# Kernel optimization log

Hardware: AMD Instinct MI355X
Metric: run time of the kernel (lower is better)

Reference implementation:

```python
import jax, jax.numpy as jnp
import numpy as np

B, N, D = 4, 1024, 1024
H, DK, DV = 8, 128, 128
EPS = 1e-6


def setup_inputs() -> dict:
    key = jax.random.key(0)
    ks = jax.random.split(key, 16)
    s = 0.02
    return {
        "q_time": jax.random.normal(ks[0], (B, N, D), jnp.float32),
        "k_time": jax.random.normal(ks[1], (B, N, D), jnp.float32),
        "q_feature": jax.random.normal(ks[2], (B, N, D), jnp.float32),
        "k_feature": jax.random.normal(ks[3], (B, N, D), jnp.float32),
        "v": jax.random.normal(ks[4], (B, N, D), jnp.float32),
        "attn_mask": jax.random.randint(ks[5], (B, N, N), 0, 2, jnp.int32),
        "w_qs_time": jax.random.normal(ks[6], (H * DK, D), jnp.float32) * s,
        "w_ks_time": jax.random.normal(ks[7], (H * DK, D), jnp.float32) * s,
        "w_qs_feature": jax.random.normal(ks[8], (H * DV, D), jnp.float32) * s,
        "w_ks_feature": jax.random.normal(ks[9], (H * DV, D), jnp.float32) * s,
        "w_vs": jax.random.normal(ks[10], (H * DV, D), jnp.float32) * s,
        "w_fc": jax.random.normal(ks[11], (D, H * DV), jnp.float32) * s,
        "ln_gamma": jnp.ones((D,), jnp.float32),
        "ln_beta": jnp.zeros((D,), jnp.float32),
    }


def reference(q_time, k_time, q_feature, k_feature, v, attn_mask,
              w_qs_time, w_ks_time, w_qs_feature, w_ks_feature, w_vs,
              w_fc, ln_gamma, ln_beta):
    temp = DK ** 0.5
    residual = v

    def proj(x, w, d):
        # [B,N,D] @ [D, H*d] -> [B,H,N,d]
        return (x @ w.T).reshape(B, N, H, d).transpose(0, 2, 1, 3)

    qt = proj(q_time, w_qs_time, DK)
    kt = proj(k_time, w_ks_time, DK)
    qf = proj(q_feature, w_qs_feature, DV)
    kf = proj(k_feature, w_ks_feature, DV)
    vv = proj(v, w_vs, DV)

    # time attention: [B,H,N,N]
    attn_time = jnp.einsum('bhnd,bhmd->bhnm', qt / temp, kt)
    attn_time = jnp.where(attn_mask[:, None, :, :] == 0, -1e9, attn_time)
    attn_time = jax.nn.softmax(attn_time, axis=-1)

    # feature attention: q_feature^T @ k_feature -> [B,H,DV,DV]
    attn_feature = jnp.einsum('bhnd,bhne->bhde', qf / temp, kf)
    attn_feature = jax.nn.softmax(attn_feature, axis=-1)

    # chained matmuls: (attn_time @ v) @ attn_feature -> [B,H,N,DV]
    out = jnp.einsum('bhnm,bhmd->bhnd', attn_time, vv)
    out = jnp.einsum('bhnd,bhde->bhne', out, attn_feature)

    out = out.transpose(0, 2, 1, 3).reshape(B, N, H * DV)
    out = out @ w_fc.T + residual  # dropout = identity (eval)

    mean = jnp.mean(out, axis=-1, keepdims=True)
    var = jnp.var(out, axis=-1, keepdims=True)
    out = (out - mean) / jnp.sqrt(var + EPS) * ln_gamma + ln_beta
    return out, attn_time, attn_feature
```

## Files before the change

### kernel.cpp

```cpp
#include <hip/hip_runtime.h>
#include <hip/hip_bf16.h>
#include <cstdint>
#include <cstddef>

typedef unsigned short u16;
typedef unsigned int u32;
typedef short v8s __attribute__((ext_vector_type(8)));
typedef float v4f __attribute__((ext_vector_type(4)));
typedef __hip_bfloat16 bf16;

#define PROJ_ELEMS  4194304ull
#define AT_ELEMS    33554432ull
#define INV_TEMP    0.08838834764831845f

#define GLOBAL_AS __attribute__((address_space(1)))
#define LDS_AS    __attribute__((address_space(3)))

__device__ __forceinline__ void store_out(float* p, float v) { *p = v; }
__device__ __forceinline__ void store_out(bf16* p, float v) { *p = __float2bfloat16(v); }

__device__ __forceinline__ v8s load8f(const float* p) {
    const float4 a = *(const float4*)p;
    const float4 b = *(const float4*)(p + 4);
    v8s r;
    bf16 t;
    t = __float2bfloat16(a.x); r[0] = *(const short*)&t;
    t = __float2bfloat16(a.y); r[1] = *(const short*)&t;
    t = __float2bfloat16(a.z); r[2] = *(const short*)&t;
    t = __float2bfloat16(a.w); r[3] = *(const short*)&t;
    t = __float2bfloat16(b.x); r[4] = *(const short*)&t;
    t = __float2bfloat16(b.y); r[5] = *(const short*)&t;
    t = __float2bfloat16(b.z); r[6] = *(const short*)&t;
    t = __float2bfloat16(b.w); r[7] = *(const short*)&t;
    return r;
}

template <typename AT, typename OutT>
__device__ __forceinline__ void gemm_core(
    const AT* __restrict__ Ab, const u16* __restrict__ Bb, OutT* __restrict__ Cb,
    int K, int lda, int ldb, int ldc, float alpha, int m0, int n0)
{
    __shared__ __align__(16) u16 sA[128][32];
    __shared__ __align__(16) u16 sB[128][32];

    const int tid  = threadIdx.x;
    const int lane = tid & 63;
    const int wid  = tid >> 6;
    const int wm = (wid >> 1) * 64;
    const int wn = (wid & 1) * 64;
    const int quad = lane >> 4;
    const int l16  = lane & 15;

    v4f acc[4][4];
    #pragma unroll
    for (int i = 0; i < 4; ++i)
        #pragma unroll
        for (int j = 0; j < 4; ++j)
            acc[i][j] = (v4f){0.f, 0.f, 0.f, 0.f};

    for (int k0 = 0; k0 < K; k0 += 32) {
        #pragma unroll
        for (int it = 0; it < 2; ++it) {
            const int slot = tid + it * 256;
            const int row  = slot >> 2;
            const int cg   = (slot & 3) << 3;
            __builtin_amdgcn_global_load_lds(
                (const GLOBAL_AS void*)(Bb + (size_t)(n0 + row) * (size_t)ldb + (size_t)(k0 + cg)),
                (LDS_AS void*)((char*)&sB[0][0] + slot * 16), 16, 0, 0);
            if constexpr (sizeof(AT) == 2) {
                __builtin_amdgcn_global_load_lds(
                    (const GLOBAL_AS void*)((const u16*)Ab + (size_t)(m0 + row) * (size_t)lda + (size_t)(k0 + cg)),
                    (LDS_AS void*)((char*)&sA[0][0] + slot * 16), 16, 0, 0);
            } else {
                *(v8s*)&sA[row][cg] =
                    load8f((const float*)Ab + (size_t)(m0 + row) * (size_t)lda + (size_t)(k0 + cg));
            }
        }
        __syncthreads();

        v8s af[4], bfr[4];
        #pragma unroll
        for (int i = 0; i < 4; ++i) {
            af[i]  = *(const v8s*)&sA[wm + i * 16 + l16][quad * 8];
            bfr[i] = *(const v8s*)&sB[wn + i * 16 + l16][quad * 8];
        }
        #pragma unroll
        for (int i = 0; i < 4; ++i)
            #pragma unroll
            for (int j = 0; j < 4; ++j)
                acc[i][j] = __builtin_amdgcn_mfma_f32_16x16x32_bf16(af[i], bfr[j], acc[i][j], 0, 0, 0);
        __syncthreads();
    }

    #pragma unroll
    for (int i = 0; i < 4; ++i) {
        int rbase = m0 + wm + i * 16 + quad * 4;
        #pragma unroll
        for (int j = 0; j < 4; ++j) {
            int gcol = n0 + wn + j * 16 + l16;
            #pragma unroll
            for (int r = 0; r < 4; ++r)
                store_out(&Cb[(size_t)(rbase + r) * (size_t)ldc + (size_t)gcol],
                          acc[i][j][r] * alpha);
        }
    }
}

template <typename AT, typename OutT>
__global__ __launch_bounds__(256, 3)
void gemm_fast(const AT* __restrict__ A, const u16* __restrict__ B, OutT* __restrict__ C,
               int K, int lda, int ldb, int ldc, int batDiv,
               long long sAo, long long sAi, long long sBo, long long sBi,
               long long sCo, long long sCi, float alpha, int swz)
{
    const int z  = blockIdx.z;
    const int zo = z / batDiv;
    const int zi = z - zo * batDiv;
    int bx, by;
    if (swz) {
        const int flat = blockIdx.x + (blockIdx.y << 3);
        const int xcd = flat & 7, slt = flat >> 3;
        by = xcd + ((slt >> 3) << 3);
        bx = slt & 7;
    } else {
        bx = blockIdx.x; by = blockIdx.y;
    }
    gemm_core<AT, OutT>(A + (size_t)zo * (size_t)sAo + (size_t)zi * (size_t)sAi,
                        B + (size_t)zo * (size_t)sBo + (size_t)zi * (size_t)sBi,
                        C + (size_t)zo * (size_t)sCo + (size_t)zi * (size_t)sCi,
                        K, lda, ldb, ldc, alpha, by * 128, bx * 128);
}

struct P5 { const u16* a[5]; };
__global__ __launch_bounds__(256, 3)
void gemm_proj5(P5 As, const u16* __restrict__ W, u16* __restrict__ C)
{
    const int fid = blockIdx.x + (blockIdx.y << 3) + (blockIdx.z << 8);
    const int xcd = fid & 7, s = fid >> 3;
    const int p = ((s >> 3) << 3) + xcd;
    const int bx = s & 7;
    const int by = p & 31;
    const int z  = p >> 5;
    gemm_core<u16, bf16>(As.a[z], W + (size_t)z * 1048576ull,
                         (bf16*)(C + (size_t)z * PROJ_ELEMS),
                         1024, 1024, 1024, 1024, 1.f, by * 128, bx * 128);
}

__global__ __launch_bounds__(256, 3)
void gemm_feat_sk(const u16* __restrict__ qfT, const u16* __restrict__ kfT, float* __restrict__ Fp)
{
    const int kc = blockIdx.x, z = blockIdx.y;
    gemm_core<u16, float>(qfT + (size_t)z * 131072ull + (size_t)kc * 128ull,
                          kfT + (size_t)z * 131072ull + (size_t)kc * 128ull,
                          Fp + ((size_t)kc * 32 + z) * 16384ull,
                          128, 1024, 1024, 128, INV_TEMP, 0, 0);
}

struct CP11 { const float* p[11]; };

__global__ __launch_bounds__(256)
void cvt_all(CP11 ps, u16* __restrict__ actDst, u16* __restrict__ wDst)
{
    const int z = blockIdx.z;
    const int nblk = (z < 5) ? 2048 : 512;
    if (blockIdx.x >= nblk) return;
    const float* s = ps.p[z];
    u16* d = (z < 5) ? (actDst + (size_t)z * PROJ_ELEMS)
                     : (wDst + (size_t)(z - 5) * 1048576ull);
    const int i = (blockIdx.x * 256 + threadIdx.x) * 8;
    *(v8s*)(d + i) = load8f(s + i);
}

__global__ __launch_bounds__(256)
void mask_pack(const int* __restrict__ mask, u32* __restrict__ mb)
{
    const int w = blockIdx.x * 256 + threadIdx.x;
    const int* src = mask + (size_t)w * 32ull;
    u32 bits = 0;
    #pragma unroll
    for (int i = 0; i < 32; i += 4) {
        int4 v = *(const int4*)(src + i);
        bits |= (u32)(v.x != 0) << i;
        bits |= (u32)(v.y != 0) << (i + 1);
        bits |= (u32)(v.z != 0) << (i + 2);
        bits |= (u32)(v.w != 0) << (i + 3);
    }
    mb[w] = bits;
}

struct T3 { const u16* in[3]; u16* out[3]; };
__global__ __launch_bounds__(256)
void transpose3(T3 t3)
{
    __shared__ u16 tile[32][33];
    const int sel = blockIdx.z >> 5;
    const int z   = blockIdx.z & 31;
    const int b = z >> 3, h = z & 7;
    const u16* ib = t3.in[sel] + (size_t)b * 1048576ull + (size_t)h * 128ull;
    u16* ob = t3.out[sel] + (size_t)z * 131072ull;
    const int m0 = blockIdx.x * 32;
    const int d0 = blockIdx.y * 32;
    const int tx = threadIdx.x;
    const int ty = threadIdx.y;
    #pragma unroll
    for (int i = 0; i < 4; ++i)
        tile[ty + i * 8][tx] = ib[(size_t)(m0 + ty + i * 8) * 1024ull + (size_t)(d0 + tx)];
    __syncthreads();
    #pragma unroll
    for (int i = 0; i < 4; ++i)
        ob[(size_t)(d0 + ty + i * 8) * 1024ull + (size_t)(m0 + tx)] = tile[tx][ty + i * 8];
}

__global__ __launch_bounds__(512, 2)
void fused_attn(const u16* __restrict__ qt, const u16* __restrict__ kt,
                const u16* __restrict__ vvT, const u32* __restrict__ mb,
                float* __restrict__ oAT, u16* __restrict__ opv)
{
    __shared__ __align__(16) u16 sQ[4][128][32];
    __shared__ __align__(16) u16 sT[2][4][128][32];
    __shared__ __align__(16) u16 sP[4][128][40];
    __shared__ u32 smw[2][128][4];

    const int flat = blockIdx.x + (blockIdx.y << 3);
    const int xcd = flat & 7, slt = flat >> 3;
    const int z  = xcd + ((slt >> 3) << 3);
    const int m0 = (slt & 7) << 7;

    const int b = z >> 3, h = z & 7;
    const u16* qb = qt + (size_t)b * 1048576ull + (size_t)h * 128ull;
    const u16* kb = kt + (size_t)b * 1048576ull + (size_t)h * 128ull;
    const u16* vb = vvT + (size_t)z * 131072ull;
    float* Ob = oAT + (size_t)z * 1048576ull;
    const u32* mbb = mb + (size_t)b * 32768ull;

    const int tid = threadIdx.x;
    const int lane = tid & 63, wid = tid >> 6;
    const int quad = lane >> 4, l16 = lane & 15;
    const int wm = wid << 4;

    auto stK = [&](int nt, int buf) {
        #pragma unroll
        for (int it = 0; it < 4; ++it) {
            const int s2 = tid + it * 512;
            const int ks = s2 >> 9, row = (s2 >> 2) & 127, cg = (s2 & 3) << 3;
            __builtin_amdgcn_global_load_lds(
                (const GLOBAL_AS void*)(kb + (size_t)(nt * 128 + row) * 1024ull + ks * 32 + cg),
                (LDS_AS void*)((char*)&sT[buf][0][0][0] + s2 * 16), 16, 0, 0);
        }
    };
    auto stV = [&](int nt, int buf) {
        #pragma unroll
        for (int it = 0; it < 4; ++it) {
            const int s2 = tid + it * 512;
            const int ks = s2 >> 9, row = (s2 >> 2) & 127, cg = (s2 & 3) << 3;
            __builtin_amdgcn_global_load_lds(
                (const GLOBAL_AS void*)(vb + (size_t)row * 1024ull + nt * 128 + ks * 32 + cg),
                (LDS_AS void*)((char*)&sT[buf][0][0][0] + s2 * 16), 16, 0, 0);
        }
    };
    auto stM = [&](int nt, int buf) {
        const int W = tid;
        __builtin_amdgcn_global_load_lds(
            (const GLOBAL_AS void*)(mbb + (size_t)(m0 + (W >> 2)) * 32ull + nt * 4 + (W & 3)),
            (LDS_AS void*)((char*)&smw[buf][0][0] + W * 4), 4, 0, 0);
    };

    #pragma unroll
    for (int it = 0; it < 4; ++it) {
        const int s2 = tid + it * 512;
        const int ks = s2 >> 9, row = (s2 >> 2) & 127, cg = (s2 & 3) << 3;
        __builtin_amdgcn_global_load_lds(
            (const GLOBAL_AS void*)(qb + (size_t)(m0 + row) * 1024ull + ks * 32 + cg),
            (LDS_AS void*)((char*)&sQ[0][0][0] + s2 * 16), 16, 0, 0);
    }
    stK(0, 0); stM(0, 0);

    float Mreg[4], Lreg[4];
    #pragma unroll
    for (int x = 0; x < 4; ++x) { Mreg[x] = -3.0e38f; Lreg[x] = 0.f; }

    int bufA = 0, mcur = 0;
    for (int nt = 0; nt < 8; ++nt) {
        stK((nt + 1) & 7, bufA ^ 1);
        stM((nt + 1) & 7, mcur ^ 1);
        asm volatile("s_waitcnt vmcnt(5)" ::: "memory");
        __builtin_amdgcn_s_barrier();
        __builtin_amdgcn_sched_barrier(0);

        v4f acc[8];
        #pragma unroll
        for (int j = 0; j < 8; ++j)
            acc[j] = (v4f){0.f, 0.f, 0.f, 0.f};
        #pragma unroll
        for (int ks = 0; ks < 4; ++ks) {
            const v8s aq = *(const v8s*)&sQ[ks][wm + l16][quad * 8];
            v8s bk[8];
            #pragma unroll
            for (int j = 0; j < 8; ++j)
                bk[j] = *(const v8s*)&sT[bufA][ks][j * 16 + l16][quad * 8];
            #pragma unroll
            for (int j = 0; j < 8; ++j)
                acc[j] = __builtin_amdgcn_mfma_f32_16x16x32_bf16(aq, bk[j], acc[j], 0, 0, 0);
        }

        #pragma unroll
        for (int r = 0; r < 4; ++r) {
            const int rowl = wm + quad * 4 + r;
            const u32 mw0 = smw[mcur][rowl][0];
            const u32 mw1 = smw[mcur][rowl][1];
            const u32 mw2 = smw[mcur][rowl][2];
            const u32 mw3 = smw[mcur][rowl][3];
            float sv[8];
            float tmax = -3.0e38f;
            #pragma unroll
            for (int j = 0; j < 8; ++j) {
                const u32 word = (j < 2) ? mw0 : (j < 4) ? mw1 : (j < 6) ? mw2 : mw3;
                const int bit = ((j & 1) << 4) + l16;
                float s = acc[j][r] * INV_TEMP;
                s = ((word >> bit) & 1u) ? s : -1e9f;
                sv[j] = s;
                tmax = fmaxf(tmax, s);
            }
            #pragma unroll
            for (int m = 1; m <= 8; m <<= 1)
                tmax = fmaxf(tmax, __shfl_xor(tmax, m));
            const float Mo = Mreg[r];
            const float Mn = fmaxf(Mo, tmax);
            float t = 0.f;
            #pragma unroll
            for (int j = 0; j < 8; ++j)
                t += __expf(sv[j] - Mn);
            #pragma unroll
            for (int m = 1; m <= 8; m <<= 1)
                t += __shfl_xor(t, m);
            Lreg[r] = Lreg[r] * __expf(Mo - Mn) + t;
            Mreg[r] = Mn;
        }

        asm volatile("s_waitcnt lgkmcnt(0)" ::: "memory");
        __builtin_amdgcn_s_barrier();
        __builtin_amdgcn_sched_barrier(0);
        bufA ^= 1; mcur ^= 1;
    }

    float IL[4];
    #pragma unroll
    for (int x = 0; x < 4; ++x) IL[x] = 1.f / Lreg[x];

    const int BK = bufA;
    const int BV = BK ^ 1;

    v4f pacc[8];
    #pragma unroll
    for (int j = 0; j < 8; ++j)
        pacc[j] = (v4f){0.f, 0.f, 0.f, 0.f};

    for (int nt = 0; nt < 8; ++nt) {
        stV(nt, BV);
        if (nt == 0) {
            asm volatile("s_waitcnt vmcnt(4)" ::: "memory");
        } else {
            asm volatile("s_waitcnt vmcnt(36)" ::: "memory");
        }
        __builtin_amdgcn_s_barrier();
        __builtin_amdgcn_sched_barrier(0);

        v4f acc[8];
        #pragma unroll
        for (int j = 0; j < 8; ++j)
            acc[j] = (v4f){0.f, 0.f, 0.f, 0.f};
        #pragma unroll
        for (int ks = 0; ks < 4; ++ks) {
            const v8s aq = *(const v8s*)&sQ[ks][wm + l16][quad * 8];
            v8s bk[8];
            #pragma unroll
            for (int j = 0; j < 8; ++j)
                bk[j] = *(const v8s*)&sT[BK][ks][j * 16 + l16][quad * 8];
            #pragma unroll
            for (int j = 0; j < 8; ++j)
                acc[j] = __builtin_amdgcn_mfma_f32_16x16x32_bf16(aq, bk[j], acc[j], 0, 0, 0);
        }

        asm volatile("s_waitcnt lgkmcnt(0)" ::: "memory");
        __builtin_amdgcn_s_barrier();
        __builtin_amdgcn_sched_barrier(0);

        if (nt < 7) {
            stK(nt + 1, BK);
            stM(nt + 1, mcur ^ 1);
            asm volatile("s_waitcnt vmcnt(5)" ::: "memory");
        } else {
            asm volatile("s_waitcnt vmcnt(0)" ::: "memory");
        }

        #pragma unroll
        for (int r = 0; r < 4; ++r) {
            const int rowl = wm + quad * 4 + r;
            const u32 mw0 = smw[mcur][rowl][0];
            const u32 mw1 = smw[mcur][rowl][1];
            const u32 mw2 = smw[mcur][rowl][2];
            const u32 mw3 = smw[mcur][rowl][3];
            float* orow = Ob + (size_t)(m0 + rowl) * 1024ull + nt * 128;
            #pragma unroll
            for (int j = 0; j < 8; ++j) {
                const u32 word = (j < 2) ? mw0 : (j < 4) ? mw1 : (j < 6) ? mw2 : mw3;
                const int bit = ((j & 1) << 4) + l16;
                float s = acc[j][r] * INV_TEMP;
                s = ((word >> bit) & 1u) ? s : -1e9f;
                const float p = __expf(s - Mreg[r]) * IL[r];
                orow[j * 16 + l16] = p;
                bf16 pb = __float2bfloat16(p);
                sP[j >> 1][rowl][((j & 1) << 4) + l16] = *(const u16*)&pb;
            }
        }

        asm volatile("s_waitcnt lgkmcnt(0)" ::: "memory");
        __builtin_amdgcn_s_barrier();
        __builtin_amdgcn_sched_barrier(0);

        #pragma unroll
        for (int ks = 0; ks < 4; ++ks) {
            const v8s ap = *(const v8s*)&sP[ks][wm + l16][quad * 8];
            v8s bv[8];
            #pragma unroll
            for (int j = 0; j < 8; ++j)
                bv[j] = *(const v8s*)&sT[BV][ks][j * 16 + l16][quad * 8];
            #pragma unroll
            for (int j = 0; j < 8; ++j)
                pacc[j] = __builtin_amdgcn_mfma_f32_16x16x32_bf16(ap, bv[j], pacc[j], 0, 0, 0);
        }

        asm volatile("s_waitcnt lgkmcnt(0)" ::: "memory");
        __builtin_amdgcn_s_barrier();
        __builtin_amdgcn_sched_barrier(0);
        mcur ^= 1;
    }

    u16* opvB = opv + (size_t)z * 131072ull;
    const int rbase = m0 + wm + quad * 4;
    #pragma unroll
    for (int j = 0; j < 8; ++j) {
        const int e = j * 16 + l16;
        #pragma unroll
        for (int r = 0; r < 4; ++r) {
            bf16 t = __float2bfloat16(pacc[j][r]);
            opvB[(size_t)(rbase + r) * 128ull + e] = *(const u16*)&t;
        }
    }
}

__global__ __launch_bounds__(128)
void softmax_feat(const float* __restrict__ Fp, float* __restrict__ out_af, u16* __restrict__ FT)
{
    const int r = blockIdx.x;
    const int z = r >> 7, d = r & 127;
    const int e = threadIdx.x;
    float x = 0.f;
    #pragma unroll
    for (int kc = 0; kc < 8; ++kc)
        x += Fp[((size_t)kc * 32 + z) * 16384ull + (size_t)d * 128ull + e];
    float mx = x;
    #pragma unroll
    for (int o = 32; o; o >>= 1) mx = fmaxf(mx, __shfl_xor(mx, o));
    __shared__ float redm[2], reds[2];
    const int w = e >> 6;
    if ((e & 63) == 0) redm[w] = mx;
    __syncthreads();
    mx = fmaxf(redm[0], redm[1]);
    float ex = __expf(x - mx);
    float s = ex;
    #pragma unroll
    for (int o = 32; o; o >>= 1) s += __shfl_xor(s, o);
    if ((e & 63) == 0) reds[w] = s;
    __syncthreads();
    s = reds[0] + reds[1];
    float p = ex / s;
    out_af[(size_t)r * 128ull + e] = p;
    bf16 pb = __float2bfloat16(p);
    FT[(size_t)z * 16384ull + (size_t)e * 128ull + d] = *(const u16*)&pb;
}

__global__ __launch_bounds__(256)
void resid_ln(const float* __restrict__ fc, const float* __restrict__ v,
              const float* __restrict__ gamma, const float* __restrict__ beta,
              float* __restrict__ out)
{
    const int r = blockIdx.x;
    const int t = threadIdx.x;
    const float4* fr = (const float4*)(fc + (size_t)r * 1024ull);
    const float4* vr = (const float4*)(v  + (size_t)r * 1024ull);
    float4 a = fr[t], b4 = vr[t];
    float4 x = {a.x + b4.x, a.y + b4.y, a.z + b4.z, a.w + b4.w};
    float s  = x.x + x.y + x.z + x.w;
    float s2 = x.x * x.x + x.y * x.y + x.z * x.z + x.w * x.w;
    #pragma unroll
    for (int o = 32; o; o >>= 1) { s += __shfl_xor(s, o); s2 += __shfl_xor(s2, o); }
    __shared__ float rs[4], rs2[4];
    const int w = t >> 6;
    if ((t & 63) == 0) { rs[w] = s; rs2[w] = s2; }
    __syncthreads();
    s  = rs[0] + rs[1] + rs[2] + rs[3];
    s2 = rs2[0] + rs2[1] + rs2[2] + rs2[3];
    const float mean = s * (1.f / 1024.f);
    const float var  = s2 * (1.f / 1024.f) - mean * mean;
    const float rstd = rsqrtf(var + 1e-6f);
    const float4 g = ((const float4*)gamma)[t];
    const float4 bb = ((const float4*)beta)[t];
    float4 o4 = {(x.x - mean) * rstd * g.x + bb.x,
                 (x.y - mean) * rstd * g.y + bb.y,
                 (x.z - mean) * rstd * g.z + bb.z,
                 (x.w - mean) * rstd * g.w + bb.w};
    ((float4*)(out + (size_t)r * 1024ull))[t] = o4;
}

extern "C" void kernel_launch(void* const* d_in, const int* in_sizes, int n_in,
                              void* d_out, int out_size, void* d_ws, size_t ws_size,
                              hipStream_t stream)
{
    (void)in_sizes; (void)n_in; (void)out_size; (void)ws_size;
    const float* q_time    = (const float*)d_in[0];
    const float* k_time    = (const float*)d_in[1];
    const float* q_feature = (const float*)d_in[2];
    const float* k_feature = (const float*)d_in[3];
    const float* v_in      = (const float*)d_in[4];
    const int*   mask      = (const int*)d_in[5];
    const float* w_qs_t    = (const float*)d_in[6];
    const float* w_ks_t    = (const float*)d_in[7];
    const float* w_qs_f    = (const float*)d_in[8];
    const float* w_ks_f    = (const float*)d_in[9];
    const float* w_vs      = (const float*)d_in[10];
    const float* w_fc      = (const float*)d_in[11];
    const float* gamma     = (const float*)d_in[12];
    const float* beta      = (const float*)d_in[13];

    char* ws = (char*)d_ws;
    const size_t MB = 1ull << 20;
    u16*   act = (u16*)(ws + 0  * MB);
    u16*   wbf = (u16*)(ws + 40 * MB);
    u16*   qt  = (u16*)(ws + 52 * MB);
    u16*   vvT = (u16*)(ws + 0  * MB);
    u16*   qfT = (u16*)(ws + 8  * MB);
    u16*   kfT = (u16*)(ws + 16 * MB);
    u16*   FT  = (u16*)(ws + 24 * MB);
    float* Fp  = (float*)(ws + 25 * MB);
    u16*   opv = (u16*)(ws + 41 * MB);
    u16*   o2  = (u16*)(ws + 52 * MB);
    float* fc  = (float*)(ws + 60 * MB);
    u32*   mb  = (u32*)(ws + 92 * MB);
    u16*   kt  = qt + PROJ_ELEMS;
    u16*   qf  = kt + PROJ_ELEMS;
    u16*   kf  = qf + PROJ_ELEMS;
    u16*   vv  = kf + PROJ_ELEMS;
    u16*   wfc = wbf + 5ull * 1048576ull;

    float* out0 = (float*)d_out;
    float* oAT  = out0 + PROJ_ELEMS;
    float* oAF  = out0 + PROJ_ELEMS + AT_ELEMS;

    const dim3 blk(256);

    {
        CP11 ca;
        ca.p[0] = q_time; ca.p[1] = k_time; ca.p[2] = q_feature;
        ca.p[3] = k_feature; ca.p[4] = v_in;
        ca.p[5] = w_qs_t; ca.p[6] = w_ks_t; ca.p[7] = w_qs_f;
        ca.p[8] = w_ks_f; ca.p[9] = w_vs; ca.p[10] = w_fc;
        cvt_all<<<dim3(2048, 1, 11), blk, 0, stream>>>(ca, act, wbf);
        mask_pack<<<512, blk, 0, stream>>>(mask, mb);
    }

    {
        P5 ps; for (int i = 0; i < 5; ++i) ps.a[i] = act + (size_t)i * PROJ_ELEMS;
        gemm_proj5<<<dim3(8, 32, 5), blk, 0, stream>>>(ps, wbf, qt);
    }

    {
        T3 t3; t3.in[0] = vv; t3.in[1] = qf; t3.in[2] = kf;
               t3.out[0] = vvT; t3.out[1] = qfT; t3.out[2] = kfT;
        transpose3<<<dim3(32, 4, 96), dim3(32, 8, 1), 0, stream>>>(t3);
    }

    gemm_feat_sk<<<dim3(8, 32), blk, 0, stream>>>(qfT, kfT, Fp);

    softmax_feat<<<4096, 128, 0, stream>>>(Fp, oAF, FT);

    fused_attn<<<dim3(8, 32), dim3(512), 0, stream>>>(qt, kt, vvT, mb, oAT, opv);

    gemm_fast<<<dim3(1, 8, 32), blk, 0, stream>>>(opv, FT, (bf16*)o2, 128,
        128, 128, 1024, 8, 1048576LL, 131072LL, 131072LL, 16384LL, 1048576LL, 128LL, 1.f, 0);

    gemm_fast<<<dim3(8, 32, 1), blk, 0, stream>>>(o2, wfc, fc, 1024, 1024, 1024, 1024, 1,
        0LL, 0LL, 0LL, 0LL, 0LL, 0LL, 1.f, 1);

    resid_ln<<<4096, 256, 0, stream>>>(fc, v_in, gamma, beta, out0);
}
```

Baseline: 441.8 us.

## Fuse feature-attention matmul into attention kernel with smaller 64-row tiles

The fused attention kernel now uses 256-thread blocks over 64 query rows and 64-key tiles, doubling the block count. After the PV accumulation it multiplies by the feature-softmax matrix in-kernel (swizzled LDS tile) and writes o2 directly, removing a separate batched GEMM launch and the opv round trip. It also folds mask packing into the conversion kernel to save a launch. The second pass now waits for all loads (vmcnt(0)) each iteration, which may reduce load/compute overlap, and recomputes QK for more, smaller tiles.

New measurement: 446.4 us. Within noise of the previous version (+1.0%).

```diff
diff --git a/kernel.cpp b/kernel.cpp
--- a/kernel.cpp
+++ b/kernel.cpp
@@ -159,9 +159,26 @@
 struct CP11 { const float* p[11]; };
 
 __global__ __launch_bounds__(256)
-void cvt_all(CP11 ps, u16* __restrict__ actDst, u16* __restrict__ wDst)
+void cvt_all(CP11 ps, u16* __restrict__ actDst, u16* __restrict__ wDst,
+             const int* __restrict__ mask, u32* __restrict__ mb)
 {
     const int z = blockIdx.z;
+    if (z == 11) {
+        if (blockIdx.x >= 512) return;
+        const int w = blockIdx.x * 256 + threadIdx.x;
+        const int* src = mask + (size_t)w * 32ull;
+        u32 bits = 0;
+        #pragma unroll
+        for (int i = 0; i < 32; i += 4) {
+            int4 v = *(const int4*)(src + i);
+            bits |= (u32)(v.x != 0) << i;
+            bits |= (u32)(v.y != 0) << (i + 1);
+            bits |= (u32)(v.z != 0) << (i + 2);
+            bits |= (u32)(v.w != 0) << (i + 3);
+        }
+        mb[w] = bits;
+        return;
+    }
     const int nblk = (z < 5) ? 2048 : 512;
     if (blockIdx.x >= nblk) return;
     const float* s = ps.p[z];
@@ -169,23 +186,6 @@
                      : (wDst + (size_t)(z - 5) * 1048576ull);
     const int i = (blockIdx.x * 256 + threadIdx.x) * 8;
     *(v8s*)(d + i) = load8f(s + i);
-}
-
-__global__ __launch_bounds__(256)
-void mask_pack(const int* __restrict__ mask, u32* __restrict__ mb)
-{
-    const int w = blockIdx.x * 256 + threadIdx.x;
-    const int* src = mask + (size_t)w * 32ull;
-    u32 bits = 0;
-    #pragma unroll
-    for (int i = 0; i < 32; i += 4) {
-        int4 v = *(const int4*)(src + i);
-        bits |= (u32)(v.x != 0) << i;
-        bits |= (u32)(v.y != 0) << (i + 1);
-        bits |= (u32)(v.z != 0) << (i + 2);
-        bits |= (u32)(v.w != 0) << (i + 3);
-    }
-    mb[w] = bits;
 }
 
 struct T3 { const u16* in[3]; u16* out[3]; };
@@ -211,20 +211,21 @@
         ob[(size_t)(d0 + ty + i * 8) * 1024ull + (size_t)(m0 + tx)] = tile[tx][ty + i * 8];
 }
 
-__global__ __launch_bounds__(512, 2)
+__global__ __launch_bounds__(256, 2)
 void fused_attn(const u16* __restrict__ qt, const u16* __restrict__ kt,
                 const u16* __restrict__ vvT, const u32* __restrict__ mb,
-                float* __restrict__ oAT, u16* __restrict__ opv)
-{
-    __shared__ __align__(16) u16 sQ[4][128][32];
-    __shared__ __align__(16) u16 sT[2][4][128][32];
-    __shared__ __align__(16) u16 sP[4][128][40];
-    __shared__ u32 smw[2][128][4];
-
-    const int flat = blockIdx.x + (blockIdx.y << 3);
-    const int xcd = flat & 7, slt = flat >> 3;
-    const int z  = xcd + ((slt >> 3) << 3);
-    const int m0 = (slt & 7) << 7;
+                const u16* __restrict__ FTg,
+                float* __restrict__ oAT, u16* __restrict__ o2)
+{
+    __shared__ __align__(16) u16 sQ[4][64][32];
+    __shared__ __align__(16) u16 sT2[2][8192];
+    __shared__ __align__(16) u16 sP[2][64][40];
+    __shared__ u32 smw[2][64][2];
+
+    const int flat = blockIdx.x + (blockIdx.y << 4);
+    const int xcd = flat & 7, s = flat >> 3;
+    const int z  = xcd + ((s >> 4) << 3);
+    const int m0 = (s & 15) << 6;
 
     const int b = z >> 3, h = z & 7;
     const u16* qb = qt + (size_t)b * 1048576ull + (size_t)h * 128ull;
@@ -241,34 +242,34 @@
     auto stK = [&](int nt, int buf) {
         #pragma unroll
         for (int it = 0; it < 4; ++it) {
-            const int s2 = tid + it * 512;
-            const int ks = s2 >> 9, row = (s2 >> 2) & 127, cg = (s2 & 3) << 3;
+            const int s2 = tid + it * 256;
+            const int ks = s2 >> 8, row = (s2 >> 2) & 63, cg = (s2 & 3) << 3;
             __builtin_amdgcn_global_load_lds(
-                (const GLOBAL_AS void*)(kb + (size_t)(nt * 128 + row) * 1024ull + ks * 32 + cg),
-                (LDS_AS void*)((char*)&sT[buf][0][0][0] + s2 * 16), 16, 0, 0);
+                (const GLOBAL_AS void*)(kb + (size_t)(nt * 64 + row) * 1024ull + ks * 32 + cg),
+                (LDS_AS void*)((char*)&sT2[buf][0] + s2 * 16), 16, 0, 0);
         }
     };
     auto stV = [&](int nt, int buf) {
         #pragma unroll
         for (int it = 0; it < 4; ++it) {
-            const int s2 = tid + it * 512;
-            const int ks = s2 >> 9, row = (s2 >> 2) & 127, cg = (s2 & 3) << 3;
+            const int s2 = tid + it * 256;
+            const int ks2 = s2 >> 9, row = (s2 >> 2) & 127, cg = (s2 & 3) << 3;
             __builtin_amdgcn_global_load_lds(
-                (const GLOBAL_AS void*)(vb + (size_t)row * 1024ull + nt * 128 + ks * 32 + cg),
-                (LDS_AS void*)((char*)&sT[buf][0][0][0] + s2 * 16), 16, 0, 0);
+                (const GLOBAL_AS void*)(vb + (size_t)row * 1024ull + nt * 64 + ks2 * 32 + cg),
+                (LDS_AS void*)((char*)&sT2[buf][0] + s2 * 16), 16, 0, 0);
         }
     };
     auto stM = [&](int nt, int buf) {
-        const int W = tid;
+        const int W = tid & 127;
         __builtin_amdgcn_global_load_lds(
-            (const GLOBAL_AS void*)(mbb + (size_t)(m0 + (W >> 2)) * 32ull + nt * 4 + (W & 3)),
+            (const GLOBAL_AS void*)(mbb + (size_t)(m0 + (W >> 1)) * 32ull + nt * 2 + (W & 1)),
             (LDS_AS void*)((char*)&smw[buf][0][0] + W * 4), 4, 0, 0);
     };
 
     #pragma unroll
     for (int it = 0; it < 4; ++it) {
-        const int s2 = tid + it * 512;
-        const int ks = s2 >> 9, row = (s2 >> 2) & 127, cg = (s2 & 3) << 3;
+        const int s2 = tid + it * 256;
+        const int ks = s2 >> 8, row = (s2 >> 2) & 63, cg = (s2 & 3) << 3;
         __builtin_amdgcn_global_load_lds(
             (const GLOBAL_AS void*)(qb + (size_t)(m0 + row) * 1024ull + ks * 32 + cg),
             (LDS_AS void*)((char*)&sQ[0][0][0] + s2 * 16), 16, 0, 0);
@@ -280,26 +281,26 @@
     for (int x = 0; x < 4; ++x) { Mreg[x] = -3.0e38f; Lreg[x] = 0.f; }
 
     int bufA = 0, mcur = 0;
-    for (int nt = 0; nt < 8; ++nt) {
-        stK((nt + 1) & 7, bufA ^ 1);
-        stM((nt + 1) & 7, mcur ^ 1);
+    for (int nt = 0; nt < 16; ++nt) {
+        stK((nt + 1) & 15, bufA ^ 1);
+        stM((nt + 1) & 15, mcur ^ 1);
         asm volatile("s_waitcnt vmcnt(5)" ::: "memory");
         __builtin_amdgcn_s_barrier();
         __builtin_amdgcn_sched_barrier(0);
 
-        v4f acc[8];
-        #pragma unroll
-        for (int j = 0; j < 8; ++j)
+        v4f acc[4];
+        #pragma unroll
+        for (int j = 0; j < 4; ++j)
             acc[j] = (v4f){0.f, 0.f, 0.f, 0.f};
         #pragma unroll
         for (int ks = 0; ks < 4; ++ks) {
             const v8s aq = *(const v8s*)&sQ[ks][wm + l16][quad * 8];
-            v8s bk[8];
-            #pragma unroll
-            for (int j = 0; j < 8; ++j)
-                bk[j] = *(const v8s*)&sT[bufA][ks][j * 16 + l16][quad * 8];
-            #pragma unroll
-            for (int j = 0; j < 8; ++j)
+            v8s bk[4];
+            #pragma unroll
+            for (int j = 0; j < 4; ++j)
+                bk[j] = *(const v8s*)&sT2[bufA][ks * 2048 + (j * 16 + l16) * 32 + quad * 8];
+            #pragma unroll
+            for (int j = 0; j < 4; ++j)
                 acc[j] = __builtin_amdgcn_mfma_f32_16x16x32_bf16(aq, bk[j], acc[j], 0, 0, 0);
         }
 
@@ -308,18 +309,16 @@
             const int rowl = wm + quad * 4 + r;
             const u32 mw0 = smw[mcur][rowl][0];
             const u32 mw1 = smw[mcur][rowl][1];
-            const u32 mw2 = smw[mcur][rowl][2];
-            const u32 mw3 = smw[mcur][rowl][3];
-            float sv[8];
+            float sv[4];
             float tmax = -3.0e38f;
             #pragma unroll
-            for (int j = 0; j < 8; ++j) {
-                const u32 word = (j < 2) ? mw0 : (j < 4) ? mw1 : (j < 6) ? mw2 : mw3;
+            for (int j = 0; j < 4; ++j) {
+                const u32 word = (j < 2) ? mw0 : mw1;
                 const int bit = ((j & 1) << 4) + l16;
-                float s = acc[j][r] * INV_TEMP;
-                s = ((word >> bit) & 1u) ? s : -1e9f;
-                sv[j] = s;
-                tmax = fmaxf(tmax, s);
+                float sc = acc[j][r] * INV_TEMP;
+                sc = ((word >> bit) & 1u) ? sc : -1e9f;
+                sv[j] = sc;
+                tmax = fmaxf(tmax, sc);
             }
             #pragma unroll
             for (int m = 1; m <= 8; m <<= 1)
@@ -328,7 +327,7 @@
             const float Mn = fmaxf(Mo, tmax);
             float t = 0.f;
             #pragma unroll
-            for (int j = 0; j < 8; ++j)
+            for (int j = 0; j < 4; ++j)
                 t += __expf(sv[j] - Mn);
             #pragma unroll
             for (int m = 1; m <= 8; m <<= 1)
@@ -343,54 +342,37 @@
         bufA ^= 1; mcur ^= 1;
     }
 
+    const int BK = 0, BV = 1;
+    stV(0, BV);
+
     float IL[4];
     #pragma unroll
     for (int x = 0; x < 4; ++x) IL[x] = 1.f / Lreg[x];
-
-    const int BK = bufA;
-    const int BV = BK ^ 1;
 
     v4f pacc[8];
     #pragma unroll
     for (int j = 0; j < 8; ++j)
         pacc[j] = (v4f){0.f, 0.f, 0.f, 0.f};
 
-    for (int nt = 0; nt < 8; ++nt) {
-        stV(nt, BV);
-        if (nt == 0) {
-            asm volatile("s_waitcnt vmcnt(4)" ::: "memory");
-        } else {
-            asm volatile("s_waitcnt vmcnt(36)" ::: "memory");
-        }
+    for (int nt = 0; nt < 16; ++nt) {
+        asm volatile("s_waitcnt vmcnt(0)" ::: "memory");
         __builtin_amdgcn_s_barrier();
         __builtin_amdgcn_sched_barrier(0);
 
-        v4f acc[8];
-        #pragma unroll
-        for (int j = 0; j < 8; ++j)
+        v4f acc[4];
+        #pragma unroll
+        for (int j = 0; j < 4; ++j)
             acc[j] = (v4f){0.f, 0.f, 0.f, 0.f};
         #pragma unroll
         for (int ks = 0; ks < 4; ++ks) {
             const v8s aq = *(const v8s*)&sQ[ks][wm + l16][quad * 8];
-            v8s bk[8];
-            #pragma unroll
-            for (int j = 0; j < 8; ++j)
-                bk[j] = *(const v8s*)&sT[BK][ks][j * 16 + l16][quad * 8];
-            #pragma unroll
-            for (int j = 0; j < 8; ++j)
+            v8s bk[4];
+            #pragma unroll
+            for (int j = 0; j < 4; ++j)
+                bk[j] = *(const v8s*)&sT2[BK][ks * 2048 + (j * 16 + l16) * 32 + quad * 8];
+            #pragma unroll
+            for (int j = 0; j < 4; ++j)
                 acc[j] = __builtin_amdgcn_mfma_f32_16x16x32_bf16(aq, bk[j], acc[j], 0, 0, 0);
-        }
-
-        asm volatile("s_waitcnt lgkmcnt(0)" ::: "memory");
-        __builtin_amdgcn_s_barrier();
-        __builtin_amdgcn_sched_barrier(0);
-
-        if (nt < 7) {
-            stK(nt + 1, BK);
-            stM(nt + 1, mcur ^ 1);
-            asm volatile("s_waitcnt vmcnt(5)" ::: "memory");
-        } else {
-            asm volatile("s_waitcnt vmcnt(0)" ::: "memory");
         }
 
         #pragma unroll
@@ -398,19 +380,18 @@
             const int rowl = wm + quad * 4 + r;
             const u32 mw0 = smw[mcur][rowl][0];
             const u32 mw1 = smw[mcur][rowl][1];
-            const u32 mw2 = smw[mcur][rowl][2];
-            const u32 mw3 = smw[mcur][rowl][3];
-            float* orow = Ob + (size_t)(m0 + rowl) * 1024ull + nt * 128;
-            #pragma unroll
-            for (int j = 0; j < 8; ++j) {
-                const u32 word = (j < 2) ? mw0 : (j < 4) ? mw1 : (j < 6) ? mw2 : mw3;
+            float* orow = Ob + (size_t)(m0 + rowl) * 1024ull + nt * 64;
+            #pragma unroll
+            for (int j = 0; j < 4; ++j) {
+                const u32 word = (j < 2) ? mw0 : mw1;
                 const int bit = ((j & 1) << 4) + l16;
-                float s = acc[j][r] * INV_TEMP;
-                s = ((word >> bit) & 1u) ? s : -1e9f;
-                const float p = __expf(s - Mreg[r]) * IL[r];
+                float sc = acc[j][r] * INV_TEMP;
+                sc = ((word >> bit) & 1u) ? sc : -1e9f;
+                const float p = __expf(sc - Mreg[r]) * IL[r];
                 orow[j * 16 + l16] = p;
                 bf16 pb = __float2bfloat16(p);
-                sP[j >> 1][rowl][((j & 1) << 4) + l16] = *(const u16*)&pb;
+                const int c = j * 16 + l16;
+                sP[c >> 5][rowl][c & 31] = *(const u16*)&pb;
             }
         }
 
@@ -418,13 +399,15 @@
         __builtin_amdgcn_s_barrier();
         __builtin_amdgcn_sched_barrier(0);
 
-        #pragma unroll
-        for (int ks = 0; ks < 4; ++ks) {
-            const v8s ap = *(const v8s*)&sP[ks][wm + l16][quad * 8];
+        if (nt < 15) { stK(nt + 1, BK); stM(nt + 1, mcur ^ 1); }
+
+        #pragma unroll
+        for (int ks2 = 0; ks2 < 2; ++ks2) {
+            const v8s ap = *(const v8s*)&sP[ks2][wm + l16][quad * 8];
             v8s bv[8];
             #pragma unroll
             for (int j = 0; j < 8; ++j)
-                bv[j] = *(const v8s*)&sT[BV][ks][j * 16 + l16][quad * 8];
+                bv[j] = *(const v8s*)&sT2[BV][ks2 * 4096 + (j * 16 + l16) * 32 + quad * 8];
             #pragma unroll
             for (int j = 0; j < 8; ++j)
                 pacc[j] = __builtin_amdgcn_mfma_f32_16x16x32_bf16(ap, bv[j], pacc[j], 0, 0, 0);
@@ -433,18 +416,61 @@
         asm volatile("s_waitcnt lgkmcnt(0)" ::: "memory");
         __builtin_amdgcn_s_barrier();
         __builtin_amdgcn_sched_barrier(0);
+
+        if (nt < 15) stV(nt + 1, BV);
         mcur ^= 1;
     }
 
-    u16* opvB = opv + (size_t)z * 131072ull;
-    const int rbase = m0 + wm + quad * 4;
+    u16* sPVp = &sQ[0][0][0];
+    u16* sFTp = &sT2[0][0];
+    const u16* FTz = FTg + (size_t)z * 16384ull;
+
     #pragma unroll
     for (int j = 0; j < 8; ++j) {
-        const int e = j * 16 + l16;
+        const int c = j * 16 + l16;
         #pragma unroll
         for (int r = 0; r < 4; ++r) {
-            bf16 t = __float2bfloat16(pacc[j][r]);
-            opvB[(size_t)(rbase + r) * 128ull + e] = *(const u16*)&t;
+            const int rowl = wm + quad * 4 + r;
+            bf16 pb = __float2bfloat16(pacc[j][r]);
+            sPVp[(c >> 5) * 2048 + rowl * 32 + (c & 31)] = *(const u16*)&pb;
+        }
+    }
+    #pragma unroll
+    for (int rep = 0; rep < 8; ++rep) {
+        const int grp = tid + rep * 256;
+        const int row = grp >> 4;
+        v8s v = *(const v8s*)(FTz + (size_t)grp * 8ull);
+        *(v8s*)((char*)sFTp + ((grp * 16) ^ ((row & 7) << 4))) = v;
+    }
+    asm volatile("s_waitcnt lgkmcnt(0)" ::: "memory");
+    __builtin_amdgcn_s_barrier();
+    __builtin_amdgcn_sched_barrier(0);
+
+    v4f o2a[8];
+    #pragma unroll
+    for (int j = 0; j < 8; ++j)
+        o2a[j] = (v4f){0.f, 0.f, 0.f, 0.f};
+    #pragma unroll
+    for (int ks = 0; ks < 4; ++ks) {
+        const v8s ap2 = *(const v8s*)&sPVp[ks * 2048 + (wm + l16) * 32 + quad * 8];
+        #pragma unroll
+        for (int j = 0; j < 8; ++j) {
+            const int rowf = j * 16 + l16;
+            const v8s bft = *(const v8s*)((char*)sFTp +
+                ((rowf * 256 + ks * 64 + quad * 16) ^ ((rowf & 7) << 4)));
+            o2a[j] = __builtin_amdgcn_mfma_f32_16x16x32_bf16(ap2, bft, o2a[j], 0, 0, 0);
+        }
+    }
+
+    u16* o2B = o2 + (size_t)b * 1048576ull + (size_t)h * 128ull;
+    #pragma unroll
+    for (int j = 0; j < 8; ++j) {
+        const int c = j * 16 + l16;
+        #pragma unroll
+        for (int r = 0; r < 4; ++r) {
+            const int m = m0 + wm + quad * 4 + r;
+            bf16 t = __float2bfloat16(o2a[j][r]);
+            o2B[(size_t)m * 1024ull + c] = *(const u16*)&t;
         }
     }
 }
@@ -543,8 +569,7 @@
     u16*   kfT = (u16*)(ws + 16 * MB);
     u16*   FT  = (u16*)(ws + 24 * MB);
     float* Fp  = (float*)(ws + 25 * MB);
-    u16*   opv = (u16*)(ws + 41 * MB);
-    u16*   o2  = (u16*)(ws + 52 * MB);
+    u16*   o2  = (u16*)(ws + 41 * MB);
     float* fc  = (float*)(ws + 60 * MB);
     u32*   mb  = (u32*)(ws + 92 * MB);
     u16*   kt  = qt + PROJ_ELEMS;
@@ -565,8 +590,7 @@
         ca.p[3] = k_feature; ca.p[4] = v_in;
         ca.p[5] = w_qs_t; ca.p[6] = w_ks_t; ca.p[7] = w_qs_f;
         ca.p[8] = w_ks_f; ca.p[9] = w_vs; ca.p[10] = w_fc;
-        cvt_all<<<dim3(2048, 1, 11), blk, 0, stream>>>(ca, act, wbf);
-        mask_pack<<<512, blk, 0, stream>>>(mask, mb);
+        cvt_all<<<dim3(2048, 1, 12), blk, 0, stream>>>(ca, act, wbf, mask, mb);
     }
 
     {
@@ -584,10 +608,7 @@
 
     softmax_feat<<<4096, 128, 0, stream>>>(Fp, oAF, FT);
 
-    fused_attn<<<dim3(8, 32), dim3(512), 0, stream>>>(qt, kt, vvT, mb, oAT, opv);
-
-    gemm_fast<<<dim3(1, 8, 32), blk, 0, stream>>>(opv, FT, (bf16*)o2, 128,
-        128, 128, 1024, 8, 1048576LL, 131072LL, 131072LL, 16384LL, 1048576LL, 128LL, 1.f, 0);
+    fused_attn<<<dim3(16, 32), blk, 0, stream>>>(qt, kt, vvT, mb, FT, oAT, o2);
 
     gemm_fast<<<dim3(8, 32, 1), blk, 0, stream>>>(o2, wfc, fc, 1024, 1024, 1024, 1024, 1,
         0LL, 0LL, 0LL, 0LL, 0LL, 0LL, 1.f, 1);
```

## Fuse feature-attention matmul into attention epilogue and merge mask packing into conversion

Applied to the files above, without the earlier changes.

The attention kernel's epilogue now stages its P@V tile in shared memory, loads the transposed feature-softmax matrix with an XOR swizzle, and runs the second chained matmul in place. It writes the result straight into the [B,N,H*DV] layout the FC GEMM reads. This removes one gemm_fast launch and the round trip of the opv intermediate through global memory. The mask bit-packing is also folded into the conversion kernel as an extra grid slice, which saves another launch. The cost is extra LDS traffic and a barrier at the end of the attention kernel, and it reuses the sQ/sT buffers after the main loop.

Result: no change. 434.3 us (-1.7%).

```diff
diff --git a/kernel.cpp b/kernel.cpp
--- a/kernel.cpp
+++ b/kernel.cpp
@@ -159,9 +159,26 @@
 struct CP11 { const float* p[11]; };
 
 __global__ __launch_bounds__(256)
-void cvt_all(CP11 ps, u16* __restrict__ actDst, u16* __restrict__ wDst)
+void cvt_all(CP11 ps, u16* __restrict__ actDst, u16* __restrict__ wDst,
+             const int* __restrict__ mask, u32* __restrict__ mb)
 {
     const int z = blockIdx.z;
+    if (z == 11) {
+        if (blockIdx.x >= 512) return;
+        const int w = blockIdx.x * 256 + threadIdx.x;
+        const int* src = mask + (size_t)w * 32ull;
+        u32 bits = 0;
+        #pragma unroll
+        for (int i = 0; i < 32; i += 4) {
+            int4 v = *(const int4*)(src + i);
+            bits |= (u32)(v.x != 0) << i;
+            bits |= (u32)(v.y != 0) << (i + 1);
+            bits |= (u32)(v.z != 0) << (i + 2);
+            bits |= (u32)(v.w != 0) << (i + 3);
+        }
+        mb[w] = bits;
+        return;
+    }
     const int nblk = (z < 5) ? 2048 : 512;
     if (blockIdx.x >= nblk) return;
     const float* s = ps.p[z];
@@ -169,23 +186,6 @@
                      : (wDst + (size_t)(z - 5) * 1048576ull);
     const int i = (blockIdx.x * 256 + threadIdx.x) * 8;
     *(v8s*)(d + i) = load8f(s + i);
-}
-
-__global__ __launch_bounds__(256)
-void mask_pack(const int* __restrict__ mask, u32* __restrict__ mb)
-{
-    const int w = blockIdx.x * 256 + threadIdx.x;
-    const int* src = mask + (size_t)w * 32ull;
-    u32 bits = 0;
-    #pragma unroll
-    for (int i = 0; i < 32; i += 4) {
-        int4 v = *(const int4*)(src + i);
-        bits |= (u32)(v.x != 0) << i;
-        bits |= (u32)(v.y != 0) << (i + 1);
-        bits |= (u32)(v.z != 0) << (i + 2);
-        bits |= (u32)(v.w != 0) << (i + 3);
-    }
-    mb[w] = bits;
 }
 
 struct T3 { const u16* in[3]; u16* out[3]; };
@@ -214,7 +214,8 @@
 __global__ __launch_bounds__(512, 2)
 void fused_attn(const u16* __restrict__ qt, const u16* __restrict__ kt,
                 const u16* __restrict__ vvT, const u32* __restrict__ mb,
-                float* __restrict__ oAT, u16* __restrict__ opv)
+                const u16* __restrict__ FTg,
+                float* __restrict__ oAT, u16* __restrict__ o2)
 {
     __shared__ __align__(16) u16 sQ[4][128][32];
     __shared__ __align__(16) u16 sT[2][4][128][32];
@@ -436,15 +437,56 @@
         mcur ^= 1;
     }
 
-    u16* opvB = opv + (size_t)z * 131072ull;
-    const int rbase = m0 + wm + quad * 4;
+    u16* sPVp = &sQ[0][0][0];
+    u16* sFTp = &sT[0][0][0][0];
+    const u16* FTz = FTg + (size_t)z * 16384ull;
+
     #pragma unroll
     for (int j = 0; j < 8; ++j) {
-        const int e = j * 16 + l16;
+        const int c = j * 16 + l16;
         #pragma unroll
         for (int r = 0; r < 4; ++r) {
-            bf16 t = __float2bfloat16(pacc[j][r]);
-            opvB[(size_t)(rbase + r) * 128ull + e] = *(const u16*)&t;
+            const int rowl = wm + quad * 4 + r;
+            bf16 pb = __float2bfloat16(pacc[j][r]);
+            sPVp[(c >> 5) * 4096 + rowl * 32 + (c & 31)] = *(const u16*)&pb;
+        }
+    }
+    #pragma unroll
+    for (int rep = 0; rep < 4; ++rep) {
+        const int grp = tid + rep * 512;
+        const int row = grp >> 4;
+        v8s v = *(const v8s*)(FTz + (size_t)grp * 8ull);
+        *(v8s*)((char*)sFTp + ((grp * 16) ^ ((row & 7) << 4))) = v;
+    }
+    asm volatile("s_waitcnt lgkmcnt(0)" ::: "memory");
+    __builtin_amdgcn_s_barrier();
+    __builtin_amdgcn_sched_barrier(0);
+
+    v4f o2a[8];
+    #pragma unroll
+    for (int j = 0; j < 8; ++j)
+        o2a[j] = (v4f){0.f, 0.f, 0.f, 0.f};
+    #pragma unroll
+    for (int ks = 0; ks < 4; ++ks) {
+        const v8s ap2 = *(const v8s*)&sPVp[ks * 4096 + (wm + l16) * 32 + quad * 8];
+        #pragma unroll
+        for (int j = 0; j < 8; ++j) {
+            const int rowf = j * 16 + l16;
+            const v8s bft = *(const v8s*)((char*)sFTp +
+                ((rowf * 256 + ks * 64 + quad * 16) ^ ((rowf & 7) << 4)));
+            o2a[j] = __builtin_amdgcn_mfma_f32_16x16x32_bf16(ap2, bft, o2a[j], 0, 0, 0);
+        }
+    }
+
+    u16* o2B = o2 + (size_t)b * 1048576ull + (size_t)h * 128ull;
+    #pragma unroll
+    for (int j = 0; j < 8; ++j) {
+        const int c = j * 16 + l16;
+        #pragma unroll
+        for (int r = 0; r < 4; ++r) {
+            const int m = m0 + wm + quad * 4 + r;
+            bf16 t = __float2bfloat16(o2a[j][r]);
+            o2B[(size_t)m * 1024ull + c] = *(const u16*)&t;
         }
     }
 }
@@ -543,8 +585,7 @@
     u16*   kfT = (u16*)(ws + 16 * MB);
     u16*   FT  = (u16*)(ws + 24 * MB);
     float* Fp  = (float*)(ws + 25 * MB);
-    u16*   opv = (u16*)(ws + 41 * MB);
-    u16*   o2  = (u16*)(ws + 52 * MB);
+    u16*   o2  = (u16*)(ws + 41 * MB);
     float* fc  = (float*)(ws + 60 * MB);
     u32*   mb  = (u32*)(ws + 92 * MB);
     u16*   kt  = qt + PROJ_ELEMS;
@@ -565,8 +606,7 @@
         ca.p[3] = k_feature; ca.p[4] = v_in;
         ca.p[5] = w_qs_t; ca.p[6] = w_ks_t; ca.p[7] = w_qs_f;
         ca.p[8] = w_ks_f; ca.p[9] = w_vs; ca.p[10] = w_fc;
-        cvt_all<<<dim3(2048, 1, 11), blk, 0, stream>>>(ca, act, wbf);
-        mask_pack<<<512, blk, 0, stream>>>(mask, mb);
+        cvt_all<<<dim3(2048, 1, 12), blk, 0, stream>>>(ca, act, wbf, mask, mb);
     }
 
     {
@@ -584,10 +624,7 @@
 
     softmax_feat<<<4096, 128, 0, stream>>>(Fp, oAF, FT);
 
-    fused_attn<<<dim3(8, 32), dim3(512), 0, stream>>>(qt, kt, vvT, mb, oAT, opv);
-
-    gemm_fast<<<dim3(1, 8, 32), blk, 0, stream>>>(opv, FT, (bf16*)o2, 128,
-        128, 128, 1024, 8, 1048576LL, 131072LL, 131072LL, 16384LL, 1048576LL, 128LL, 1.f, 0);
+    fused_attn<<<dim3(8, 32), dim3(512), 0, stream>>>(qt, kt, vvT, mb, FT, oAT, o2);
 
     gemm_fast<<<dim3(8, 32, 1), blk, 0, stream>>>(o2, wfc, fc, 1024, 1024, 1024, 1024, 1,
         0LL, 0LL, 0LL, 0LL, 0LL, 0LL, 1.f, 1);
```
